# Optimization experiments

Measured on AMD Instinct MI355X. Metric: run time of the kernel, lower is better.

Reference implementation:

```python
import jax, jax.numpy as jnp
import numpy as np

B, S, E = 2, 2048, 2048
H, DH = 16, 128          # n_head, head_dim
ROT = 32                 # rotary_dim (partial RoPE)
MP = 8                   # mp_num in original forward
MASKED_BIAS = -1e9


def setup_inputs() -> dict:
    key = jax.random.key(0)
    k1, k2, k3 = jax.random.split(key, 3)
    hidden_states = jax.random.normal(k1, (B, S, E), dtype=jnp.float32)
    W_qkv = jax.random.normal(k2, (3 * E, E), dtype=jnp.float32) * (E ** -0.5)
    W_out = jax.random.normal(k3, (E, E), dtype=jnp.float32) * (E ** -0.5)
    return {"hidden_states": hidden_states, "W_qkv": W_qkv, "W_out": W_out}


def _rope_sincos(seq_len, rot_dim, dtype):
    inv_freq = 1.0 / (10000.0 ** (jnp.arange(0, rot_dim, 2, dtype=jnp.float32) / rot_dim))
    ang = jnp.arange(seq_len, dtype=jnp.float32)[:, None] * inv_freq[None, :]  # [S, R/2]
    return jnp.sin(ang).astype(dtype), jnp.cos(ang).astype(dtype)


def _apply_rope(x, sin, cos):
    # x: [B,S,H,R]; sin/cos: [S,R/2] -> repeat_interleave(2) -> [S,R]
    sin2 = jnp.repeat(sin, 2, axis=-1)[None, :, None, :]
    cos2 = jnp.repeat(cos, 2, axis=-1)[None, :, None, :]
    x1 = x[..., ::2]
    x2 = x[..., 1::2]
    rot = jnp.stack((-x2, x1), axis=-1).reshape(x.shape)  # rotate_every_two
    return x * cos2 + rot * sin2


def reference(hidden_states, W_qkv, W_out):
    b, s, e = hidden_states.shape
    # qkv_proj (no bias): torch Linear does x @ W^T
    qkv = jnp.einsum('bse,fe->bsf', hidden_states, W_qkv)          # [B,S,3E]
    qkv = qkv.reshape(b, s, MP, 3 * e // MP)
    q, k, v = jnp.split(qkv, 3, axis=-1)                            # each [B,S,MP,E/MP]
    # _split_heads: flatten mp dim, re-split into heads
    q = q.reshape(b, s, H, DH)
    k = k.reshape(b, s, H, DH)
    v = v.reshape(b, s, H, DH)
    # partial rotary on first ROT dims (q,k in [B,S,H,DH] layout)
    sin, cos = _rope_sincos(s, ROT, hidden_states.dtype)
    q = jnp.concatenate([_apply_rope(q[..., :ROT], sin, cos), q[..., ROT:]], axis=-1)
    k = jnp.concatenate([_apply_rope(k[..., :ROT], sin, cos), k[..., ROT:]], axis=-1)
    # attention: scores / sqrt(DH), causal masked_fill(-1e9), softmax, AV
    scale = jnp.sqrt(jnp.asarray(DH, dtype=jnp.float32)).astype(hidden_states.dtype)
    scores = jnp.einsum('bqhd,bkhd->bhqk', q, k) / scale            # [B,H,S,S]
    causal = jnp.tril(jnp.ones((s, s), dtype=bool))
    scores = jnp.where(causal[None, None], scores, jnp.asarray(MASKED_BIAS, scores.dtype))
    attn = jax.nn.softmax(scores, axis=-1)
    out = jnp.einsum('bhqk,bkhd->bqhd', attn, v)                    # [B,S,H,DH]
    out = out.reshape(b, s, e)
    return jnp.einsum('bse,fe->bsf', out, W_out)                    # out_proj
```

## Files before the change

kernel.cpp:

```cpp
#include <hip/hip_runtime.h>
#include <hip/hip_bf16.h>
#include <cstdint>
#include <cstddef>

using bf16 = __hip_bfloat16;
using short4v = __attribute__((ext_vector_type(4))) short;
using short8 = __attribute__((ext_vector_type(8))) short;
using floatx4 = __attribute__((ext_vector_type(4))) float;

#define MFMA_BF16(A, B, C) __builtin_amdgcn_mfma_f32_16x16x32_bf16((A), (B), (C), 0, 0, 0)

__device__ inline short bf16_bits(float x) {
  bf16 v = __float2bfloat16(x);
  short r;
  __builtin_memcpy(&r, &v, 2);
  return r;
}

__device__ inline void store_c(bf16* p, float v) { *p = __float2bfloat16(v); }
__device__ inline void store_c(float* p, float v) { *p = v; }

__global__ __launch_bounds__(256) void f32_to_bf16_kernel(
    const float* __restrict__ src, bf16* __restrict__ dst, int n8) {
  const int i = blockIdx.x * 256 + threadIdx.x;
  if (i >= n8) return;
  const float4 a = ((const float4*)src)[2 * i];
  const float4 b = ((const float4*)src)[2 * i + 1];
  short8 r;
  r[0] = bf16_bits(a.x); r[1] = bf16_bits(a.y); r[2] = bf16_bits(a.z); r[3] = bf16_bits(a.w);
  r[4] = bf16_bits(b.x); r[5] = bf16_bits(b.y); r[6] = bf16_bits(b.z); r[7] = bf16_bits(b.w);
  *(short8*)(dst + (size_t)i * 8) = r;
}

template <typename TC>
__global__ __launch_bounds__(256) void gemm_bt_async(
    const bf16* __restrict__ A, const bf16* __restrict__ B, TC* __restrict__ C,
    int ldc, int K) {
  __shared__ bf16 As[128 * 64];
  __shared__ bf16 Bs[128 * 64];
  const int tid = threadIdx.x;
  const int lane = tid & 63;
  const int wave = tid >> 6;
  const int lrow = lane & 15;
  const int quad = lane >> 4;
  const int wm = (wave >> 1) * 64;
  const int wn = (wave & 1) * 64;
  const int tm = blockIdx.y * 128;
  const int tn = blockIdx.x * 128;

  const int srow = tid >> 3;
  const int scl = tid & 7;

  floatx4 acc[4][4] = {};

  for (int k0 = 0; k0 < K; k0 += 64) {
    __syncthreads();
#pragma unroll
    for (int r = 0; r < 4; ++r) {
      const int row = r * 32 + srow;
      const int scg = scl ^ (row & 7);
      __builtin_amdgcn_global_load_lds(
          (const __attribute__((address_space(1))) void*)(A + (size_t)(tm + row) * K + k0 + scg * 8),
          (__attribute__((address_space(3))) void*)(As + row * 64 + scl * 8), 16, 0, 0);
    }
#pragma unroll
    for (int r = 0; r < 4; ++r) {
      const int row = r * 32 + srow;
      const int scg = scl ^ (row & 7);
      __builtin_amdgcn_global_load_lds(
          (const __attribute__((address_space(1))) void*)(B + (size_t)(tn + row) * K + k0 + scg * 8),
          (__attribute__((address_space(3))) void*)(Bs + row * 64 + scl * 8), 16, 0, 0);
    }
    __syncthreads();

#pragma unroll
    for (int kk = 0; kk < 2; ++kk) {
      short8 af[4], bfr[4];
#pragma unroll
      for (int i = 0; i < 4; ++i) {
        const int ra = wm + i * 16 + lrow;
        const int rb = wn + i * 16 + lrow;
        af[i] = *(const short8*)&As[ra * 64 + (((kk * 4 + quad) ^ (ra & 7)) * 8)];
        bfr[i] = *(const short8*)&Bs[rb * 64 + (((kk * 4 + quad) ^ (rb & 7)) * 8)];
      }
#pragma unroll
      for (int i = 0; i < 4; ++i)
#pragma unroll
        for (int j = 0; j < 4; ++j)
          acc[i][j] = MFMA_BF16(af[i], bfr[j], acc[i][j]);
    }
  }

#pragma unroll
  for (int i = 0; i < 4; ++i)
#pragma unroll
    for (int j = 0; j < 4; ++j)
#pragma unroll
      for (int r = 0; r < 4; ++r) {
        const int row = tm + wm + i * 16 + quad * 4 + r;
        const int col = tn + wn + j * 16 + lrow;
        store_c(&C[(size_t)row * ldc + col], acc[i][j][r]);
      }
}

__global__ __launch_bounds__(256) void gemm_abf16_bf32(
    const bf16* __restrict__ A, const float* __restrict__ B, float* __restrict__ C,
    int ldc, int K) {
  __shared__ bf16 As[128 * 64];
  __shared__ bf16 Bs[128 * 64];
  const int tid = threadIdx.x;
  const int lane = tid & 63;
  const int wave = tid >> 6;
  const int lrow = lane & 15;
  const int quad = lane >> 4;
  const int wm = (wave >> 1) * 64;
  const int wn = (wave & 1) * 64;
  const int tm = blockIdx.y * 128;
  const int tn = blockIdx.x * 128;

  const int srow = tid >> 3;
  const int scl = tid & 7;
  const int c16 = tid & 15;
  const int br0 = tid >> 4;

  floatx4 acc[4][4] = {};
  float4 breg[8];
#pragma unroll
  for (int r = 0; r < 8; ++r)
    breg[r] = *(const float4*)(B + (size_t)(tn + r * 16 + br0) * K + c16 * 4);

  for (int k0 = 0; k0 < K; k0 += 64) {
    __syncthreads();
#pragma unroll
    for (int r = 0; r < 4; ++r) {
      const int row = r * 32 + srow;
      const int scg = scl ^ (row & 7);
      __builtin_amdgcn_global_load_lds(
          (const __attribute__((address_space(1))) void*)(A + (size_t)(tm + row) * K + k0 + scg * 8),
          (__attribute__((address_space(3))) void*)(As + row * 64 + scl * 8), 16, 0, 0);
    }
#pragma unroll
    for (int r = 0; r < 8; ++r) {
      const int row = r * 16 + br0;
      short4v sv;
      sv[0] = bf16_bits(breg[r].x); sv[1] = bf16_bits(breg[r].y);
      sv[2] = bf16_bits(breg[r].z); sv[3] = bf16_bits(breg[r].w);
      *(short4v*)&Bs[row * 64 + (((c16 >> 1) ^ (row & 7)) * 8) + (c16 & 1) * 4] = sv;
    }
    __syncthreads();
    if (k0 + 64 < K) {
#pragma unroll
      for (int r = 0; r < 8; ++r)
        breg[r] = *(const float4*)(B + (size_t)(tn + r * 16 + br0) * K + k0 + 64 + c16 * 4);
    }

#pragma unroll
    for (int kk = 0; kk < 2; ++kk) {
      short8 af[4], bfr[4];
#pragma unroll
      for (int i = 0; i < 4; ++i) {
        const int ra = wm + i * 16 + lrow;
        const int rb = wn + i * 16 + lrow;
        af[i] = *(const short8*)&As[ra * 64 + (((kk * 4 + quad) ^ (ra & 7)) * 8)];
        bfr[i] = *(const short8*)&Bs[rb * 64 + (((kk * 4 + quad) ^ (rb & 7)) * 8)];
      }
#pragma unroll
      for (int i = 0; i < 4; ++i)
#pragma unroll
        for (int j = 0; j < 4; ++j)
          acc[i][j] = MFMA_BF16(af[i], bfr[j], acc[i][j]);
    }
  }

#pragma unroll
  for (int i = 0; i < 4; ++i)
#pragma unroll
    for (int j = 0; j < 4; ++j)
#pragma unroll
      for (int r = 0; r < 4; ++r) {
        const int row = tm + wm + i * 16 + quad * 4 + r;
        const int col = tn + wn + j * 16 + lrow;
        C[(size_t)row * ldc + col] = acc[i][j][r];
      }
}

__global__ void rope_kernel(bf16* __restrict__ qkv) {
  const int idx = blockIdx.x * 256 + threadIdx.x;
  const int i = idx & 15;
  int t = idx >> 4;
  const int qk = t & 1;
  t >>= 1;
  const int h = t & 15;
  t >>= 4;
  const int s = t & 2047;
  bf16* p = qkv + (size_t)t * 6144 + (h >> 1) * 768 + (h & 1) * 128 + qk * 256 + 2 * i;
  const float x0 = __bfloat162float(p[0]);
  const float x1 = __bfloat162float(p[1]);
  const float inv = powf(10000.f, -(float)(2 * i) / 32.f);
  const float ang = (float)s * inv;
  float sn, cs;
  sincosf(ang, &sn, &cs);
  p[0] = __float2bfloat16(x0 * cs - x1 * sn);
  p[1] = __float2bfloat16(x1 * cs + x0 * sn);
}

__global__ __launch_bounds__(256) void attn_flash_pair(
    const bf16* __restrict__ qkv, bf16* __restrict__ out) {
  __shared__ short Ks[16 * 64 * 8];
  __shared__ short Vs[128 * 64];
  __shared__ short Ps[128 * 64];
  const int tid = threadIdx.x;
  const int wave = tid >> 6;
  const int lane = tid & 63;
  const int lrow = lane & 15;
  const int quad = lane >> 4;
  const int h = blockIdx.y;
  const int b = blockIdx.z;
  const size_t SROW = 6144;
  const bf16* base = qkv + (size_t)b * 2048 * SROW;
  const int qoff = (h >> 1) * 768 + (h & 1) * 128;
  const int koff = qoff + 256;
  const int voff = qoff + 512;
  const float scale = 0.088388347648318447f;

  const int sr = tid >> 2;
  const int sq = tid & 3;

  const bf16* kbase = base + (size_t)sr * SROW + koff + sq * 32;
  const bf16* vbase = base + (size_t)sr * SROW + voff + sq * 8;

  short8 kv[4], vv[4];
#pragma unroll
  for (int j = 0; j < 4; ++j) kv[j] = *(const short8*)(kbase + j * 8);
#pragma unroll
  for (int i = 0; i < 4; ++i) vv[i] = *(const short8*)(vbase + i * 32);

  for (int phase = 0; phase < 2; ++phase) {
    const int qb = phase ? (15 - (int)blockIdx.x) : (int)blockIdx.x;

    short8 qf[2][4];
#pragma unroll
    for (int rt = 0; rt < 2; ++rt) {
      const bf16* qp =
          base + (size_t)(qb * 128 + wave * 32 + rt * 16 + lrow) * SROW + qoff + quad * 8;
#pragma unroll
      for (int ks = 0; ks < 4; ++ks) qf[rt][ks] = *(const short8*)(qp + ks * 32);
    }

    floatx4 o[2][8] = {};
    float m_i[8], l_i[8];
#pragma unroll
    for (int i = 0; i < 8; ++i) {
      m_i[i] = -1e30f;
      l_i[i] = 0.f;
    }

    const int kb_end = 2 * qb + 2;
    for (int kb = 0; kb < kb_end; ++kb) {
      __syncthreads();

#pragma unroll
      for (int j = 0; j < 4; ++j) *(short8*)&Ks[((sq * 4 + j) * 64 + sr) * 8] = kv[j];
      {
        const int kc = sr >> 3;
        const int si = sr & 7;
#pragma unroll
        for (int i = 0; i < 4; ++i) {
          const int dbase = sq * 8 + i * 32;
          const int cc = kc ^ ((dbase >> 3) & 7);
#pragma unroll
          for (int j = 0; j < 8; ++j) {
            Vs[(dbase + j) * 64 + ((cc ^ j) * 8) + si] = vv[i][j];
          }
        }
      }
      __syncthreads();

      {
        const bool last = (kb + 1 == kb_end);
        const bool pf = !last || (phase == 0);
        const int nkb = !last ? kb + 1 : 0;
        if (pf) {
          const size_t off = (size_t)nkb * 64 * SROW;
#pragma unroll
          for (int j = 0; j < 4; ++j) kv[j] = *(const short8*)(kbase + off + j * 8);
#pragma unroll
          for (int i = 0; i < 4; ++i) vv[i] = *(const short8*)(vbase + off + i * 32);
        }
      }

      floatx4 sc[2][4] = {};
      __builtin_amdgcn_s_setprio(1);
#pragma unroll
      for (int ks = 0; ks < 4; ++ks) {
        short8 bfr[4];
#pragma unroll
        for (int ct = 0; ct < 4; ++ct)
          bfr[ct] = *(const short8*)&Ks[((ks * 4 + quad) * 64 + ct * 16 + lrow) * 8];
#pragma unroll
        for (int rt = 0; rt < 2; ++rt)
#pragma unroll
          for (int ct = 0; ct < 4; ++ct)
            sc[rt][ct] = MFMA_BF16(qf[rt][ks], bfr[ct], sc[rt][ct]);
      }
      __builtin_amdgcn_s_setprio(0);

      const int wr0 = qb * 128 + wave * 32;
      const bool diag = (kb * 64 + 63 > wr0);
#pragma unroll
      for (int rt = 0; rt < 2; ++rt)
#pragma unroll
        for (int r = 0; r < 4; ++r) {
          const int idx = rt * 4 + r;
          const int row_g = wr0 + rt * 16 + quad * 4 + r;
          float mx = -1e30f;
#pragma unroll
          for (int ct = 0; ct < 4; ++ct) {
            float v = sc[rt][ct][r] * scale;
            if (diag) {
              const int col_g = kb * 64 + ct * 16 + lrow;
              if (col_g > row_g) v = -1e9f;
            }
            sc[rt][ct][r] = v;
            mx = fmaxf(mx, v);
          }
#pragma unroll
          for (int off = 1; off < 16; off <<= 1) mx = fmaxf(mx, __shfl_xor(mx, off, 64));
          const float mnew = fmaxf(m_i[idx], mx);
          const float alpha = __expf(m_i[idx] - mnew);
          m_i[idx] = mnew;
          float rs = 0.f;
#pragma unroll
          for (int ct = 0; ct < 4; ++ct) {
            const float p = __expf(sc[rt][ct][r] - mnew);
            sc[rt][ct][r] = p;
            rs += p;
          }
#pragma unroll
          for (int off = 1; off < 16; off <<= 1) rs += __shfl_xor(rs, off, 64);
          l_i[idx] = l_i[idx] * alpha + rs;
#pragma unroll
          for (int dt = 0; dt < 8; ++dt) o[rt][dt][r] *= alpha;
        }

#pragma unroll
      for (int rt = 0; rt < 2; ++rt)
#pragma unroll
        for (int ct = 0; ct < 4; ++ct)
#pragma unroll
          for (int r = 0; r < 4; ++r) {
            const int row_l = wave * 32 + rt * 16 + quad * 4 + r;
            const int skgrp = ct * 2 + (lrow >> 3);
            const int cc = skgrp ^ (row_l & 7);
            Ps[row_l * 64 + cc * 8 + (lrow & 7)] = bf16_bits(sc[rt][ct][r]);
          }

      __builtin_amdgcn_s_setprio(1);
#pragma unroll
      for (int ks = 0; ks < 2; ++ks) {
        short8 af[2], bfr[8];
#pragma unroll
        for (int rt = 0; rt < 2; ++rt) {
          const int row = wave * 32 + rt * 16 + lrow;
          const int cc = (ks * 4 + quad) ^ (row & 7);
          af[rt] = *(const short8*)&Ps[row * 64 + cc * 8];
        }
#pragma unroll
        for (int dt = 0; dt < 8; ++dt) {
          const int d = dt * 16 + lrow;
          const int cc = ((ks * 4 + quad) ^ (d & 7) ^ ((d >> 3) & 7)) & 7;
          bfr[dt] = *(const short8*)&Vs[d * 64 + cc * 8];
        }
#pragma unroll
        for (int rt = 0; rt < 2; ++rt)
#pragma unroll
          for (int dt = 0; dt < 8; ++dt)
            o[rt][dt] = MFMA_BF16(af[rt], bfr[dt], o[rt][dt]);
      }
      __builtin_amdgcn_s_setprio(0);
    }

#pragma unroll
    for (int rt = 0; rt < 2; ++rt)
#pragma unroll
      for (int r = 0; r < 4; ++r) {
        const float inv_l = 1.f / l_i[rt * 4 + r];
        const int row = qb * 128 + wave * 32 + rt * 16 + quad * 4 + r;
#pragma unroll
        for (int dt = 0; dt < 8; ++dt) {
          const int d = dt * 16 + lrow;
          out[((size_t)(b * 2048 + row)) * 2048 + h * 128 + d] =
              __float2bfloat16(o[rt][dt][r] * inv_l);
        }
      }
  }
}

extern "C" void kernel_launch(void* const* d_in, const int* in_sizes, int n_in,
                              void* d_out, int out_size, void* d_ws, size_t ws_size,
                              hipStream_t stream) {
  const float* hidden = (const float*)d_in[0];
  const float* Wqkv = (const float*)d_in[1];
  const float* Wout = (const float*)d_in[2];
  float* outp = (float*)d_out;

  bf16* qkv = (bf16*)d_ws;
  bf16* flex = qkv + (size_t)4096 * 6144;
  bf16* hbf = (bf16*)d_out;

  f32_to_bf16_kernel<<<4096, 256, 0, stream>>>(hidden, hbf, 1048576);

  f32_to_bf16_kernel<<<3072, 256, 0, stream>>>(Wqkv, flex, 786432);
  gemm_bt_async<bf16><<<dim3(24, 32), 256, 0, stream>>>(hbf, flex, qkv, 6144, 2048);
  f32_to_bf16_kernel<<<3072, 256, 0, stream>>>(Wqkv + (size_t)3072 * 2048, flex, 786432);
  gemm_bt_async<bf16><<<dim3(24, 32), 256, 0, stream>>>(hbf, flex, qkv + 3072, 6144, 2048);

  rope_kernel<<<8192, 256, 0, stream>>>(qkv);

  bf16* attnout = flex;
  attn_flash_pair<<<dim3(8, 16, 2), 256, 0, stream>>>(qkv, attnout);

  gemm_abf16_bf32<<<dim3(16, 32), 256, 0, stream>>>(attnout, Wout, outp, 2048, 2048);
}
```

Baseline: 458.7 us.

## Transpose flash-attention MFMA operands so each lane owns a query row

Swaps the A/B operands in both QK^T and PV MFMAs so the accumulator is transposed and each lane holds one query row's columns in registers. Row max and sum reductions then need two cross-lane shuffles instead of four per row and eight rows, and the online-softmax state shrinks to two values per lane. P is written to LDS as packed 4-element vectors, V and P use a k-group-major LDS layout with no XOR swizzle, and the output store becomes 4-wide vectors. Removing the swizzle may add LDS bank conflicts on the V scatter and on the fragment reads.

New measurement: 434.8 us. 1.05x faster.

```diff
diff --git a/kernel.cpp b/kernel.cpp
--- a/kernel.cpp
+++ b/kernel.cpp
@@ -207,12 +207,12 @@
 __global__ __launch_bounds__(256) void attn_flash_pair(
     const bf16* __restrict__ qkv, bf16* __restrict__ out) {
   __shared__ short Ks[16 * 64 * 8];
-  __shared__ short Vs[128 * 64];
-  __shared__ short Ps[128 * 64];
+  __shared__ short Vs[8 * 128 * 8];
+  __shared__ short Ps[8 * 128 * 8];
   const int tid = threadIdx.x;
   const int wave = tid >> 6;
   const int lane = tid & 63;
-  const int lrow = lane & 15;
+  const int lq = lane & 15;
   const int quad = lane >> 4;
   const int h = blockIdx.y;
   const int b = blockIdx.z;
@@ -242,18 +242,14 @@
 #pragma unroll
     for (int rt = 0; rt < 2; ++rt) {
       const bf16* qp =
-          base + (size_t)(qb * 128 + wave * 32 + rt * 16 + lrow) * SROW + qoff + quad * 8;
+          base + (size_t)(qb * 128 + wave * 32 + rt * 16 + lq) * SROW + qoff + quad * 8;
 #pragma unroll
       for (int ks = 0; ks < 4; ++ks) qf[rt][ks] = *(const short8*)(qp + ks * 32);
     }
 
     floatx4 o[2][8] = {};
-    float m_i[8], l_i[8];
-#pragma unroll
-    for (int i = 0; i < 8; ++i) {
-      m_i[i] = -1e30f;
-      l_i[i] = 0.f;
-    }
+    float m_i[2] = {-1e30f, -1e30f};
+    float l_i[2] = {0.f, 0.f};
 
     const int kb_end = 2 * qb + 2;
     for (int kb = 0; kb < kb_end; ++kb) {
@@ -262,16 +258,12 @@
 #pragma unroll
       for (int j = 0; j < 4; ++j) *(short8*)&Ks[((sq * 4 + j) * 64 + sr) * 8] = kv[j];
       {
-        const int kc = sr >> 3;
-        const int si = sr & 7;
+        const int so = (sr >> 3) * 128, si = sr & 7;
 #pragma unroll
         for (int i = 0; i < 4; ++i) {
-          const int dbase = sq * 8 + i * 32;
-          const int cc = kc ^ ((dbase >> 3) & 7);
-#pragma unroll
-          for (int j = 0; j < 8; ++j) {
-            Vs[(dbase + j) * 64 + ((cc ^ j) * 8) + si] = vv[i][j];
-          }
+          const int d0 = sq * 8 + i * 32;
+#pragma unroll
+          for (int j = 0; j < 8; ++j) Vs[(so + d0 + j) * 8 + si] = vv[i][j];
         }
       }
       __syncthreads();
@@ -293,106 +285,105 @@
       __builtin_amdgcn_s_setprio(1);
 #pragma unroll
       for (int ks = 0; ks < 4; ++ks) {
-        short8 bfr[4];
+        short8 kf[4];
 #pragma unroll
         for (int ct = 0; ct < 4; ++ct)
-          bfr[ct] = *(const short8*)&Ks[((ks * 4 + quad) * 64 + ct * 16 + lrow) * 8];
+          kf[ct] = *(const short8*)&Ks[((ks * 4 + quad) * 64 + ct * 16 + lq) * 8];
 #pragma unroll
         for (int rt = 0; rt < 2; ++rt)
 #pragma unroll
           for (int ct = 0; ct < 4; ++ct)
-            sc[rt][ct] = MFMA_BF16(qf[rt][ks], bfr[ct], sc[rt][ct]);
+            sc[rt][ct] = MFMA_BF16(kf[ct], qf[rt][ks], sc[rt][ct]);
       }
       __builtin_amdgcn_s_setprio(0);
 
-      const int wr0 = qb * 128 + wave * 32;
-      const bool diag = (kb * 64 + 63 > wr0);
-#pragma unroll
-      for (int rt = 0; rt < 2; ++rt)
-#pragma unroll
-        for (int r = 0; r < 4; ++r) {
-          const int idx = rt * 4 + r;
-          const int row_g = wr0 + rt * 16 + quad * 4 + r;
-          float mx = -1e30f;
-#pragma unroll
-          for (int ct = 0; ct < 4; ++ct) {
+      const int qrow0 = qb * 128 + wave * 32;
+      const bool diag = (kb * 64 + 63 > qrow0);
+#pragma unroll
+      for (int rt = 0; rt < 2; ++rt) {
+        const int qg = qrow0 + rt * 16 + lq;
+#pragma unroll
+        for (int ct = 0; ct < 4; ++ct)
+#pragma unroll
+          for (int r = 0; r < 4; ++r) {
             float v = sc[rt][ct][r] * scale;
-            if (diag) {
-              const int col_g = kb * 64 + ct * 16 + lrow;
-              if (col_g > row_g) v = -1e9f;
-            }
+            if (diag && (kb * 64 + ct * 16 + quad * 4 + r) > qg) v = -1e9f;
             sc[rt][ct][r] = v;
-            mx = fmaxf(mx, v);
           }
-#pragma unroll
-          for (int off = 1; off < 16; off <<= 1) mx = fmaxf(mx, __shfl_xor(mx, off, 64));
-          const float mnew = fmaxf(m_i[idx], mx);
-          const float alpha = __expf(m_i[idx] - mnew);
-          m_i[idx] = mnew;
-          float rs = 0.f;
-#pragma unroll
-          for (int ct = 0; ct < 4; ++ct) {
-            const float p = __expf(sc[rt][ct][r] - mnew);
-            sc[rt][ct][r] = p;
-            rs += p;
-          }
-#pragma unroll
-          for (int off = 1; off < 16; off <<= 1) rs += __shfl_xor(rs, off, 64);
-          l_i[idx] = l_i[idx] * alpha + rs;
-#pragma unroll
-          for (int dt = 0; dt < 8; ++dt) o[rt][dt][r] *= alpha;
+        float c0 = fmaxf(fmaxf(sc[rt][0][0], sc[rt][0][1]), fmaxf(sc[rt][0][2], sc[rt][0][3]));
+        float c1 = fmaxf(fmaxf(sc[rt][1][0], sc[rt][1][1]), fmaxf(sc[rt][1][2], sc[rt][1][3]));
+        float c2 = fmaxf(fmaxf(sc[rt][2][0], sc[rt][2][1]), fmaxf(sc[rt][2][2], sc[rt][2][3]));
+        float c3 = fmaxf(fmaxf(sc[rt][3][0], sc[rt][3][1]), fmaxf(sc[rt][3][2], sc[rt][3][3]));
+        float mx = fmaxf(fmaxf(c0, c1), fmaxf(c2, c3));
+        mx = fmaxf(mx, __shfl_xor(mx, 16, 64));
+        mx = fmaxf(mx, __shfl_xor(mx, 32, 64));
+        const float mnew = fmaxf(m_i[rt], mx);
+        const float alpha = __expf(m_i[rt] - mnew);
+        m_i[rt] = mnew;
+        float s0 = 0.f, s1 = 0.f, s2 = 0.f, s3 = 0.f;
+#pragma unroll
+        for (int ct = 0; ct < 4; ++ct) {
+          const float p0 = __expf(sc[rt][ct][0] - mnew);
+          const float p1 = __expf(sc[rt][ct][1] - mnew);
+          const float p2 = __expf(sc[rt][ct][2] - mnew);
+          const float p3 = __expf(sc[rt][ct][3] - mnew);
+          sc[rt][ct][0] = p0; sc[rt][ct][1] = p1; sc[rt][ct][2] = p2; sc[rt][ct][3] = p3;
+          s0 += p0; s1 += p1; s2 += p2; s3 += p3;
         }
-
-#pragma unroll
-      for (int rt = 0; rt < 2; ++rt)
-#pragma unroll
-        for (int ct = 0; ct < 4; ++ct)
-#pragma unroll
-          for (int r = 0; r < 4; ++r) {
-            const int row_l = wave * 32 + rt * 16 + quad * 4 + r;
-            const int skgrp = ct * 2 + (lrow >> 3);
-            const int cc = skgrp ^ (row_l & 7);
-            Ps[row_l * 64 + cc * 8 + (lrow & 7)] = bf16_bits(sc[rt][ct][r]);
-          }
+        float rs = (s0 + s1) + (s2 + s3);
+        rs += __shfl_xor(rs, 16, 64);
+        rs += __shfl_xor(rs, 32, 64);
+        l_i[rt] = l_i[rt] * alpha + rs;
+#pragma unroll
+        for (int dt = 0; dt < 8; ++dt) {
+          o[rt][dt][0] *= alpha; o[rt][dt][1] *= alpha;
+          o[rt][dt][2] *= alpha; o[rt][dt][3] *= alpha;
+        }
+        const int prow = wave * 32 + rt * 16 + lq;
+#pragma unroll
+        for (int ct = 0; ct < 4; ++ct) {
+          short4v pv;
+          pv[0] = bf16_bits(sc[rt][ct][0]); pv[1] = bf16_bits(sc[rt][ct][1]);
+          pv[2] = bf16_bits(sc[rt][ct][2]); pv[3] = bf16_bits(sc[rt][ct][3]);
+          const int kgrp = ct * 2 + (quad >> 1);
+          *(short4v*)&Ps[(kgrp * 128 + prow) * 8 + (quad & 1) * 4] = pv;
+        }
+      }
 
       __builtin_amdgcn_s_setprio(1);
 #pragma unroll
-      for (int ks = 0; ks < 2; ++ks) {
-        short8 af[2], bfr[8];
-#pragma unroll
-        for (int rt = 0; rt < 2; ++rt) {
-          const int row = wave * 32 + rt * 16 + lrow;
-          const int cc = (ks * 4 + quad) ^ (row & 7);
-          af[rt] = *(const short8*)&Ps[row * 64 + cc * 8];
-        }
-#pragma unroll
-        for (int dt = 0; dt < 8; ++dt) {
-          const int d = dt * 16 + lrow;
-          const int cc = ((ks * 4 + quad) ^ (d & 7) ^ ((d >> 3) & 7)) & 7;
-          bfr[dt] = *(const short8*)&Vs[d * 64 + cc * 8];
-        }
+      for (int kk = 0; kk < 2; ++kk) {
+        short8 pf[2], vf[8];
 #pragma unroll
         for (int rt = 0; rt < 2; ++rt)
+          pf[rt] = *(const short8*)&Ps[((kk * 4 + quad) * 128 + wave * 32 + rt * 16 + lq) * 8];
+#pragma unroll
+        for (int dt = 0; dt < 8; ++dt)
+          vf[dt] = *(const short8*)&Vs[((kk * 4 + quad) * 128 + dt * 16 + lq) * 8];
+#pragma unroll
+        for (int rt = 0; rt < 2; ++rt)
 #pragma unroll
           for (int dt = 0; dt < 8; ++dt)
-            o[rt][dt] = MFMA_BF16(af[rt], bfr[dt], o[rt][dt]);
+            o[rt][dt] = MFMA_BF16(vf[dt], pf[rt], o[rt][dt]);
       }
       __builtin_amdgcn_s_setprio(0);
     }
 
 #pragma unroll
-    for (int rt = 0; rt < 2; ++rt)
-#pragma unroll
-      for (int r = 0; r < 4; ++r) {
-        const float inv_l = 1.f / l_i[rt * 4 + r];
-        const int row = qb * 128 + wave * 32 + rt * 16 + quad * 4 + r;
-#pragma unroll
-        for (int dt = 0; dt < 8; ++dt) {
-          const int d = dt * 16 + lrow;
-          out[((size_t)(b * 2048 + row)) * 2048 + h * 128 + d] =
-              __float2bfloat16(o[rt][dt][r] * inv_l);
-        }
-      }
+    for (int rt = 0; rt < 2; ++rt) {
+      const float inv_l = 1.f / l_i[rt];
+      const int qg = qb * 128 + wave * 32 + rt * 16 + lq;
+      bf16* op = out + ((size_t)(b * 2048 + qg)) * 2048 + h * 128 + quad * 4;
+#pragma unroll
+      for (int dt = 0; dt < 8; ++dt) {
+        short4v s4;
+        s4[0] = bf16_bits(o[rt][dt][0] * inv_l);
+        s4[1] = bf16_bits(o[rt][dt][1] * inv_l);
+        s4[2] = bf16_bits(o[rt][dt][2] * inv_l);
+        s4[3] = bf16_bits(o[rt][dt][3] * inv_l);
+        *(short4v*)(op + dt * 16) = s4;
+      }
+    }
   }
 }
 
```
